# Kernel tuning notes

Measured on AMD Instinct MI355X. Metric: run time of the kernel, lower is better.

## Reference

```python
import jax, jax.numpy as jnp
import numpy as np

N = 8192
E = 262144


def gcn_layer(x, w, row, col, edge_weight, n_nodes):
    # support = x @ W ; out = A_sparse @ support (COO spmm via segment_sum)
    support = x @ w                              # [N, d_out]
    msg = support[col] * edge_weight[:, None]    # gather + scale, [E, d_out]
    return jax.ops.segment_sum(msg, row, num_segments=n_nodes)  # [N, d_out]


def setup_inputs() -> dict:
    key = jax.random.key(0)
    k1, k2, k3, k4, k5, k6 = jax.random.split(key, 6)
    x = jax.random.normal(k1, (N, 512), dtype=jnp.float32)
    w1 = jax.random.normal(k2, (512, 256), dtype=jnp.float32) * 0.05
    w2 = jax.random.normal(k3, (256, 16), dtype=jnp.float32) * 0.05
    edge_weight = jax.random.uniform(k4, (E,), dtype=jnp.float32)
    row = jax.random.randint(k5, (E,), 0, N, dtype=jnp.int32)
    col = jax.random.randint(k6, (E,), 0, N, dtype=jnp.int32)
    return {"x": x, "w1": w1, "w2": w2, "edge_weight": edge_weight,
            "row": row, "col": col}


def reference(x, w1, w2, edge_weight, row, col):
    # gc1: dropout(identity at eval) -> linear -> spmm -> relu
    h1 = jax.nn.relu(gcn_layer(x, w1, row, col, edge_weight, N))
    # gc2: identity activation
    z = gcn_layer(h1, w2, row, col, edge_weight, N)          # [N, 16]
    # InnerProductDecoder with act = identity (dropout off at eval)
    adj = z @ z.T                                            # [N, N]
    return adj
```

## Files before the change

### kernel.cpp

```cpp
#include <hip/hip_runtime.h>

#define NN 8192
#define NE 262144
#define DIN 512
#define DH 256
#define DZ 16
#define CAP 96

typedef __attribute__((ext_vector_type(8))) short bf16x8;
typedef __attribute__((ext_vector_type(4))) float f32x4;

__device__ __forceinline__ ushort f2bf(float f) {
    uint u = __float_as_uint(f);
    uint r = (u + 0x7FFFu + ((u >> 16) & 1u)) >> 16;
    return (ushort)r;
}
__device__ __forceinline__ float bf2f(ushort h) {
    return __uint_as_float((uint)h << 16);
}

__global__ __launch_bounds__(256) void k_gemm1_scatter(
    const float* __restrict__ X, const float* __restrict__ W1,
    ushort* __restrict__ O,
    const int* __restrict__ ROW, const int* __restrict__ COL,
    const float* __restrict__ EW, int* __restrict__ count,
    int* __restrict__ col_s, float* __restrict__ w_s) {
    __shared__ ushort As[32][72];
    __shared__ ushort Bs[256][72];
    int t = threadIdx.x;
    {
        int gid0 = blockIdx.x * 256 + t;
#pragma unroll
        for (int it = 0; it < 4; ++it) {
            int e = gid0 + it * 65536;
            int r = ROW[e];
            int slot = atomicAdd(&count[r], 1);
            if (slot < CAP) {
                col_s[r * CAP + slot] = COL[e];
                w_s[r * CAP + slot]   = EW[e];
            }
        }
    }
    int wave = t >> 6, lane = t & 63;
    int m0 = blockIdx.x * 32;
    int fr = lane & 15, fg = lane >> 4;
    int ar = t >> 3, ac = (t & 7) * 8;
    f32x4 acc[2][4] = {};
    for (int k0 = 0; k0 < DIN; k0 += 64) {
        __syncthreads();
        {
            const float* xp = &X[(size_t)(m0 + ar) * DIN + k0 + ac];
            float4 f0 = *(const float4*)&xp[0];
            float4 f1 = *(const float4*)&xp[4];
            ushort u[8] = {f2bf(f0.x), f2bf(f0.y), f2bf(f0.z), f2bf(f0.w),
                           f2bf(f1.x), f2bf(f1.y), f2bf(f1.z), f2bf(f1.w)};
            *(bf16x8*)&As[ar][ac] = *(const bf16x8*)&u[0];
        }
#pragma unroll
        for (int uix = 0; uix < 4; ++uix) {
            int u = uix * 256 + t;
            int kr = (u >> 6) * 4;
            int nc = (u & 63) * 4;
            const float* wp = &W1[(size_t)(k0 + kr) * DH + nc];
            float4 f0 = *(const float4*)&wp[0];
            float4 f1 = *(const float4*)&wp[DH];
            float4 f2 = *(const float4*)&wp[2 * DH];
            float4 f3 = *(const float4*)&wp[3 * DH];
            ushort4 p0 = {f2bf(f0.x), f2bf(f1.x), f2bf(f2.x), f2bf(f3.x)};
            ushort4 p1 = {f2bf(f0.y), f2bf(f1.y), f2bf(f2.y), f2bf(f3.y)};
            ushort4 p2 = {f2bf(f0.z), f2bf(f1.z), f2bf(f2.z), f2bf(f3.z)};
            ushort4 p3 = {f2bf(f0.w), f2bf(f1.w), f2bf(f2.w), f2bf(f3.w)};
            *(ushort4*)&Bs[nc + 0][kr] = p0;
            *(ushort4*)&Bs[nc + 1][kr] = p1;
            *(ushort4*)&Bs[nc + 2][kr] = p2;
            *(ushort4*)&Bs[nc + 3][kr] = p3;
        }
        __syncthreads();
#pragma unroll
        for (int kk = 0; kk < 2; ++kk) {
            bf16x8 af[2], bb[4];
#pragma unroll
            for (int i = 0; i < 2; ++i)
                af[i] = *(const bf16x8*)&As[i * 16 + fr][kk * 32 + fg * 8];
#pragma unroll
            for (int j = 0; j < 4; ++j)
                bb[j] = *(const bf16x8*)&Bs[wave * 64 + j * 16 + fr][kk * 32 + fg * 8];
#pragma unroll
            for (int i = 0; i < 2; ++i)
#pragma unroll
                for (int j = 0; j < 4; ++j)
                    acc[i][j] = __builtin_amdgcn_mfma_f32_16x16x32_bf16(
                        af[i], bb[j], acc[i][j], 0, 0, 0);
        }
    }
#pragma unroll
    for (int i = 0; i < 2; ++i)
#pragma unroll
        for (int j = 0; j < 4; ++j)
#pragma unroll
            for (int r = 0; r < 4; ++r)
                O[(size_t)(m0 + i * 16 + fg * 4 + r) * DH + wave * 64 + j * 16 + fr] =
                    f2bf(acc[i][j][r]);
}

__global__ __launch_bounds__(256) void k_spmm1_gemm2(const ushort* __restrict__ Sbf,
                                                     const int* __restrict__ count,
                                                     const int* __restrict__ cs,
                                                     const float* __restrict__ wsrt,
                                                     const float* __restrict__ W2,
                                                     float* __restrict__ S2) {
    __shared__ float w2s[DH * DZ];
    __shared__ float hs[2][DH];
    __shared__ int   ecs[2][CAP];
    __shared__ float ews[2][CAP];
    int t = threadIdx.x;
#pragma unroll
    for (int i = t; i < DH * DZ / 4; i += 256)
        ((float4*)w2s)[i] = ((const float4*)W2)[i];
    int sub = t >> 7;
    int ht = t & 127;
    int r = blockIdx.x * 2 + sub;
    int nv = min(count[r], CAP);
    int e0 = r * CAP;
    if (ht < nv) {
        ecs[sub][ht] = cs[e0 + ht];
        ews[sub][ht] = wsrt[e0 + ht];
    }
    float a0 = 0.f, a1 = 0.f, b0 = 0.f, b1 = 0.f;
    float c0 = 0.f, c1 = 0.f, d0 = 0.f, d1 = 0.f;
    __syncthreads();
    int e = 0;
    for (; e + 3 < nv; e += 4) {
        int k0 = ecs[sub][e], k1 = ecs[sub][e + 1], k2 = ecs[sub][e + 2], k3 = ecs[sub][e + 3];
        float w0 = ews[sub][e], w1 = ews[sub][e + 1], w2_ = ews[sub][e + 2], w3 = ews[sub][e + 3];
        uint p0 = *(const uint*)&Sbf[(size_t)k0 * DH + ht * 2];
        uint p1 = *(const uint*)&Sbf[(size_t)k1 * DH + ht * 2];
        uint p2 = *(const uint*)&Sbf[(size_t)k2 * DH + ht * 2];
        uint p3 = *(const uint*)&Sbf[(size_t)k3 * DH + ht * 2];
        a0 += w0 * bf2f((ushort)p0); a1 += w0 * bf2f((ushort)(p0 >> 16));
        b0 += w1 * bf2f((ushort)p1); b1 += w1 * bf2f((ushort)(p1 >> 16));
        c0 += w2_ * bf2f((ushort)p2); c1 += w2_ * bf2f((ushort)(p2 >> 16));
        d0 += w3 * bf2f((ushort)p3); d1 += w3 * bf2f((ushort)(p3 >> 16));
    }
    for (; e < nv; ++e) {
        float w0 = ews[sub][e];
        uint p0 = *(const uint*)&Sbf[(size_t)ecs[sub][e] * DH + ht * 2];
        a0 += w0 * bf2f((ushort)p0); a1 += w0 * bf2f((ushort)(p0 >> 16));
    }
    float2 o;
    o.x = fmaxf(a0 + b0 + c0 + d0, 0.f);
    o.y = fmaxf(a1 + b1 + c1 + d1, 0.f);
    *(float2*)&hs[sub][ht * 2] = o;
    __syncthreads();
    int j = (t >> 3) & 15, g = t & 7;
    float acc = 0.f;
#pragma unroll
    for (int kk = 0; kk < 32; ++kk) {
        int k = g * 32 + kk;
        acc += hs[sub][k] * w2s[k * DZ + j];
    }
    acc += __shfl_xor(acc, 1);
    acc += __shfl_xor(acc, 2);
    acc += __shfl_xor(acc, 4);
    if (g == 0) S2[(size_t)r * DZ + j] = acc;
}

__global__ __launch_bounds__(256) void k_spmm2(const float* __restrict__ S2,
                                               const int* __restrict__ count,
                                               const int* __restrict__ cs,
                                               const float* __restrict__ wsrt,
                                               ushort* __restrict__ ZHi,
                                               ushort* __restrict__ ZLo) {
    int t = threadIdx.x;
    int rl = t >> 4, c = t & 15;
    int r = blockIdx.x * 16 + rl;
    int nv = min(count[r], CAP);
    int e0 = r * CAP;
    float acc = 0.f;
    for (int e = 0; e < nv; ++e)
        acc += wsrt[e0 + e] * S2[(size_t)cs[e0 + e] * DZ + c];
    ushort h = f2bf(acc);
    ZHi[(size_t)r * DZ + c] = h;
    ZLo[(size_t)r * DZ + c] = f2bf(acc - bf2f(h));
}

__global__ __launch_bounds__(256) void k_gemm3_mfma(const ushort* __restrict__ ZHi,
                                                    const ushort* __restrict__ ZLo,
                                                    float* __restrict__ O) {
    int t = threadIdx.x;
    int wave = t >> 6, lane = t & 63;
    int rb = blockIdx.y * 128 + (wave >> 1) * 64;
    int cb = blockIdx.x * 128 + (wave & 1) * 64;
    int fr = lane & 15, fg = lane >> 4;
    int ko = (fg & 1) * 8;
    const ushort* asel = (fg < 2) ? ZHi : ZLo;

    bf16x8 cpack[4], rhi[4], rlo[4];
    bf16x8 zero8 = {};
#pragma unroll
    for (int j = 0; j < 4; ++j)
        cpack[j] = *(const bf16x8*)&asel[(size_t)(cb + j * 16 + fr) * DZ + ko];
#pragma unroll
    for (int i = 0; i < 4; ++i) {
        rhi[i] = *(const bf16x8*)&ZHi[(size_t)(rb + i * 16 + fr) * DZ + ko];
        rlo[i] = (fg < 2) ? *(const bf16x8*)&ZLo[(size_t)(rb + i * 16 + fr) * DZ + ko]
                          : zero8;
    }
    f32x4 acc[4][4] = {};
#pragma unroll
    for (int i = 0; i < 4; ++i)
#pragma unroll
        for (int j = 0; j < 4; ++j) {
            acc[i][j] = __builtin_amdgcn_mfma_f32_16x16x32_bf16(cpack[j], rhi[i],
                                                                acc[i][j], 0, 0, 0);
            acc[i][j] = __builtin_amdgcn_mfma_f32_16x16x32_bf16(cpack[j], rlo[i],
                                                                acc[i][j], 0, 0, 0);
        }
#pragma unroll
    for (int i = 0; i < 4; ++i)
#pragma unroll
        for (int j = 0; j < 4; ++j)
            *(f32x4*)&O[(size_t)(rb + i * 16 + fr) * NN + cb + j * 16 + fg * 4] = acc[i][j];
}

extern "C" void kernel_launch(void* const* d_in, const int* in_sizes, int n_in,
                              void* d_out, int out_size, void* d_ws, size_t ws_size,
                              hipStream_t stream) {
    const float* x  = (const float*)d_in[0];
    const float* w1 = (const float*)d_in[1];
    const float* w2 = (const float*)d_in[2];
    const float* ew = (const float*)d_in[3];
    const int*  row = (const int*)d_in[4];
    const int*  col = (const int*)d_in[5];
    float* out = (float*)d_out;

    char* ws = (char*)d_ws;
    int*    count = (int*)ws;
    ushort* zhi   = (ushort*)(ws + 73728);
    ushort* zlo   = (ushort*)(ws + 73728 + 262144);

    char* ob = (char*)d_out;
    ushort* support1 = (ushort*)ob;
    float*  s2       = (float*)(ob + 16u * 1024 * 1024);
    int*    col_s    = (int*)(ob + 24u * 1024 * 1024);
    float*  w_s      = (float*)(ob + 28u * 1024 * 1024);

    hipMemsetAsync(count, 0, NN * sizeof(int), stream);

    k_gemm1_scatter<<<NN / 32, 256, 0, stream>>>(x, w1, support1,
                                                 row, col, ew, count, col_s, w_s);
    k_spmm1_gemm2<<<NN / 2, 256, 0, stream>>>(support1, count, col_s, w_s, w2, s2);
    k_spmm2<<<NN / 16, 256, 0, stream>>>(s2, count, col_s, w_s, zhi, zlo);
    k_gemm3_mfma<<<dim3(NN / 128, NN / 128), 256, 0, stream>>>(zhi, zlo, out);
}
```

Before: 135.9 us.

## Pre-transpose W1 to bf16, drop LDS staging in GEMM1, wave-per-row SpMM1

A new prep kernel converts W1 to a transposed bf16 copy and zeroes the edge counters, replacing the memset. GEMM1 then reads MFMA operands directly from global memory with no LDS staging or barriers, using 16-row tiles and twice as many blocks. SpMM1 assigns one wave per row with 8-byte gathers and four rows per block. The aim is to remove the per-block redundant W1 conversion and transpose plus the LDS sync overhead, at the cost of more global or L2 traffic for B fragments and an extra launch.

```diff
diff --git a/kernel.cpp b/kernel.cpp
--- a/kernel.cpp
+++ b/kernel.cpp
@@ -19,20 +19,31 @@
     return __uint_as_float((uint)h << 16);
 }
 
+__global__ void k_prep_zero(const float* __restrict__ W, ushort* __restrict__ WBf,
+                            int* __restrict__ count) {
+    int b = blockIdx.x;
+    int t = threadIdx.x;
+    if (b < 512) {
+        int o = b * 256 + t;
+        int n = o >> 9, k = o & 511;
+        WBf[o] = f2bf(W[(size_t)k * DH + n]);
+    } else {
+        count[(b - 512) * 256 + t] = 0;
+    }
+}
+
 __global__ __launch_bounds__(256) void k_gemm1_scatter(
-    const float* __restrict__ X, const float* __restrict__ W1,
+    const float* __restrict__ X, const ushort* __restrict__ W1T,
     ushort* __restrict__ O,
     const int* __restrict__ ROW, const int* __restrict__ COL,
     const float* __restrict__ EW, int* __restrict__ count,
     int* __restrict__ col_s, float* __restrict__ w_s) {
-    __shared__ ushort As[32][72];
-    __shared__ ushort Bs[256][72];
     int t = threadIdx.x;
     {
         int gid0 = blockIdx.x * 256 + t;
 #pragma unroll
-        for (int it = 0; it < 4; ++it) {
-            int e = gid0 + it * 65536;
+        for (int it = 0; it < 2; ++it) {
+            int e = gid0 + it * 131072;
             int r = ROW[e];
             int slot = atomicAdd(&count[r], 1);
             if (slot < CAP) {
@@ -42,65 +53,32 @@
         }
     }
     int wave = t >> 6, lane = t & 63;
-    int m0 = blockIdx.x * 32;
+    int m0 = blockIdx.x * 16;
     int fr = lane & 15, fg = lane >> 4;
-    int ar = t >> 3, ac = (t & 7) * 8;
-    f32x4 acc[2][4] = {};
+    f32x4 acc[4] = {};
+    const float* xrow = &X[(size_t)(m0 + fr) * DIN];
     for (int k0 = 0; k0 < DIN; k0 += 64) {
-        __syncthreads();
-        {
-            const float* xp = &X[(size_t)(m0 + ar) * DIN + k0 + ac];
+#pragma unroll
+        for (int kk = 0; kk < 2; ++kk) {
+            const float* xp = &xrow[k0 + kk * 32 + fg * 8];
             float4 f0 = *(const float4*)&xp[0];
             float4 f1 = *(const float4*)&xp[4];
-            ushort u[8] = {f2bf(f0.x), f2bf(f0.y), f2bf(f0.z), f2bf(f0.w),
-                           f2bf(f1.x), f2bf(f1.y), f2bf(f1.z), f2bf(f1.w)};
-            *(bf16x8*)&As[ar][ac] = *(const bf16x8*)&u[0];
+            ushort ua[8] = {f2bf(f0.x), f2bf(f0.y), f2bf(f0.z), f2bf(f0.w),
+                            f2bf(f1.x), f2bf(f1.y), f2bf(f1.z), f2bf(f1.w)};
+            bf16x8 af = *(const bf16x8*)&ua[0];
+#pragma unroll
+            for (int j = 0; j < 4; ++j) {
+                bf16x8 bb = *(const bf16x8*)&W1T[(size_t)(wave * 64 + j * 16 + fr) * DIN +
+                                                 k0 + kk * 32 + fg * 8];
+                acc[j] = __builtin_amdgcn_mfma_f32_16x16x32_bf16(af, bb, acc[j], 0, 0, 0);
+            }
         }
-#pragma unroll
-        for (int uix = 0; uix < 4; ++uix) {
-            int u = uix * 256 + t;
-            int kr = (u >> 6) * 4;
-            int nc = (u & 63) * 4;
-            const float* wp = &W1[(size_t)(k0 + kr) * DH + nc];
-            float4 f0 = *(const float4*)&wp[0];
-            float4 f1 = *(const float4*)&wp[DH];
-            float4 f2 = *(const float4*)&wp[2 * DH];
-            float4 f3 = *(const float4*)&wp[3 * DH];
-            ushort4 p0 = {f2bf(f0.x), f2bf(f1.x), f2bf(f2.x), f2bf(f3.x)};
-            ushort4 p1 = {f2bf(f0.y), f2bf(f1.y), f2bf(f2.y), f2bf(f3.y)};
-            ushort4 p2 = {f2bf(f0.z), f2bf(f1.z), f2bf(f2.z), f2bf(f3.z)};
-            ushort4 p3 = {f2bf(f0.w), f2bf(f1.w), f2bf(f2.w), f2bf(f3.w)};
-            *(ushort4*)&Bs[nc + 0][kr] = p0;
-            *(ushort4*)&Bs[nc + 1][kr] = p1;
-            *(ushort4*)&Bs[nc + 2][kr] = p2;
-            *(ushort4*)&Bs[nc + 3][kr] = p3;
-        }
-        __syncthreads();
-#pragma unroll
-        for (int kk = 0; kk < 2; ++kk) {
-            bf16x8 af[2], bb[4];
-#pragma unroll
-            for (int i = 0; i < 2; ++i)
-                af[i] = *(const bf16x8*)&As[i * 16 + fr][kk * 32 + fg * 8];
-#pragma unroll
-            for (int j = 0; j < 4; ++j)
-                bb[j] = *(const bf16x8*)&Bs[wave * 64 + j * 16 + fr][kk * 32 + fg * 8];
-#pragma unroll
-            for (int i = 0; i < 2; ++i)
-#pragma unroll
-                for (int j = 0; j < 4; ++j)
-                    acc[i][j] = __builtin_amdgcn_mfma_f32_16x16x32_bf16(
-                        af[i], bb[j], acc[i][j], 0, 0, 0);
-        }
-    }
-#pragma unroll
-    for (int i = 0; i < 2; ++i)
-#pragma unroll
-        for (int j = 0; j < 4; ++j)
-#pragma unroll
-            for (int r = 0; r < 4; ++r)
-                O[(size_t)(m0 + i * 16 + fg * 4 + r) * DH + wave * 64 + j * 16 + fr] =
-                    f2bf(acc[i][j][r]);
+    }
+#pragma unroll
+    for (int j = 0; j < 4; ++j)
+#pragma unroll
+        for (int r = 0; r < 4; ++r)
+            O[(size_t)(m0 + fg * 4 + r) * DH + wave * 64 + j * 16 + fr] = f2bf(acc[j][r]);
 }
 
 __global__ __launch_bounds__(256) void k_spmm1_gemm2(const ushort* __restrict__ Sbf,
@@ -110,59 +88,61 @@
                                                      const float* __restrict__ W2,
                                                      float* __restrict__ S2) {
     __shared__ float w2s[DH * DZ];
-    __shared__ float hs[2][DH];
-    __shared__ int   ecs[2][CAP];
-    __shared__ float ews[2][CAP];
+    __shared__ float hs[4][DH];
+    __shared__ int   ecs[4][CAP];
+    __shared__ float ews[4][CAP];
     int t = threadIdx.x;
 #pragma unroll
     for (int i = t; i < DH * DZ / 4; i += 256)
         ((float4*)w2s)[i] = ((const float4*)W2)[i];
-    int sub = t >> 7;
-    int ht = t & 127;
-    int r = blockIdx.x * 2 + sub;
+    int wave = t >> 6, lane = t & 63;
+    int r = blockIdx.x * 4 + wave;
     int nv = min(count[r], CAP);
     int e0 = r * CAP;
-    if (ht < nv) {
-        ecs[sub][ht] = cs[e0 + ht];
-        ews[sub][ht] = wsrt[e0 + ht];
-    }
-    float a0 = 0.f, a1 = 0.f, b0 = 0.f, b1 = 0.f;
-    float c0 = 0.f, c1 = 0.f, d0 = 0.f, d1 = 0.f;
-    __syncthreads();
+    if (lane < nv) { ecs[wave][lane] = cs[e0 + lane]; ews[wave][lane] = wsrt[e0 + lane]; }
+    int l2 = lane + 64;
+    if (l2 < nv) { ecs[wave][l2] = cs[e0 + l2]; ews[wave][l2] = wsrt[e0 + l2]; }
+    float a0[4] = {}, a1[4] = {}, a2[4] = {}, a3[4] = {};
     int e = 0;
     for (; e + 3 < nv; e += 4) {
-        int k0 = ecs[sub][e], k1 = ecs[sub][e + 1], k2 = ecs[sub][e + 2], k3 = ecs[sub][e + 3];
-        float w0 = ews[sub][e], w1 = ews[sub][e + 1], w2_ = ews[sub][e + 2], w3 = ews[sub][e + 3];
-        uint p0 = *(const uint*)&Sbf[(size_t)k0 * DH + ht * 2];
-        uint p1 = *(const uint*)&Sbf[(size_t)k1 * DH + ht * 2];
-        uint p2 = *(const uint*)&Sbf[(size_t)k2 * DH + ht * 2];
-        uint p3 = *(const uint*)&Sbf[(size_t)k3 * DH + ht * 2];
-        a0 += w0 * bf2f((ushort)p0); a1 += w0 * bf2f((ushort)(p0 >> 16));
-        b0 += w1 * bf2f((ushort)p1); b1 += w1 * bf2f((ushort)(p1 >> 16));
-        c0 += w2_ * bf2f((ushort)p2); c1 += w2_ * bf2f((ushort)(p2 >> 16));
-        d0 += w3 * bf2f((ushort)p3); d1 += w3 * bf2f((ushort)(p3 >> 16));
+        int k0 = ecs[wave][e], k1 = ecs[wave][e + 1];
+        int k2 = ecs[wave][e + 2], k3 = ecs[wave][e + 3];
+        float w0 = ews[wave][e], w1 = ews[wave][e + 1];
+        float w2_ = ews[wave][e + 2], w3 = ews[wave][e + 3];
+        uint2 p0 = *(const uint2*)&Sbf[(size_t)k0 * DH + lane * 4];
+        uint2 p1 = *(const uint2*)&Sbf[(size_t)k1 * DH + lane * 4];
+        uint2 p2 = *(const uint2*)&Sbf[(size_t)k2 * DH + lane * 4];
+        uint2 p3 = *(const uint2*)&Sbf[(size_t)k3 * DH + lane * 4];
+        a0[0] += w0 * bf2f((ushort)p0.x); a0[1] += w0 * bf2f((ushort)(p0.x >> 16));
+        a0[2] += w0 * bf2f((ushort)p0.y); a0[3] += w0 * bf2f((ushort)(p0.y >> 16));
+        a1[0] += w1 * bf2f((ushort)p1.x); a1[1] += w1 * bf2f((ushort)(p1.x >> 16));
+        a1[2] += w1 * bf2f((ushort)p1.y); a1[3] += w1 * bf2f((ushort)(p1.y >> 16));
+        a2[0] += w2_ * bf2f((ushort)p2.x); a2[1] += w2_ * bf2f((ushort)(p2.x >> 16));
+        a2[2] += w2_ * bf2f((ushort)p2.y); a2[3] += w2_ * bf2f((ushort)(p2.y >> 16));
+        a3[0] += w3 * bf2f((ushort)p3.x); a3[1] += w3 * bf2f((ushort)(p3.x >> 16));
+        a3[2] += w3 * bf2f((ushort)p3.y); a3[3] += w3 * bf2f((ushort)(p3.y >> 16));
     }
     for (; e < nv; ++e) {
-        float w0 = ews[sub][e];
-        uint p0 = *(const uint*)&Sbf[(size_t)ecs[sub][e] * DH + ht * 2];
-        a0 += w0 * bf2f((ushort)p0); a1 += w0 * bf2f((ushort)(p0 >> 16));
-    }
-    float2 o;
-    o.x = fmaxf(a0 + b0 + c0 + d0, 0.f);
-    o.y = fmaxf(a1 + b1 + c1 + d1, 0.f);
-    *(float2*)&hs[sub][ht * 2] = o;
+        float w0 = ews[wave][e];
+        uint2 p0 = *(const uint2*)&Sbf[(size_t)ecs[wave][e] * DH + lane * 4];
+        a0[0] += w0 * bf2f((ushort)p0.x); a0[1] += w0 * bf2f((ushort)(p0.x >> 16));
+        a0[2] += w0 * bf2f((ushort)p0.y); a0[3] += w0 * bf2f((ushort)(p0.y >> 16));
+    }
+    float4 h;
+    h.x = fmaxf(a0[0] + a1[0] + a2[0] + a3[0], 0.f);
+    h.y = fmaxf(a0[1] + a1[1] + a2[1] + a3[1], 0.f);
+    h.z = fmaxf(a0[2] + a1[2] + a2[2] + a3[2], 0.f);
+    h.w = fmaxf(a0[3] + a1[3] + a2[3] + a3[3], 0.f);
+    *(float4*)&hs[wave][lane * 4] = h;
     __syncthreads();
-    int j = (t >> 3) & 15, g = t & 7;
+    int jj = lane >> 2, g = lane & 3;
     float acc = 0.f;
-#pragma unroll
-    for (int kk = 0; kk < 32; ++kk) {
-        int k = g * 32 + kk;
-        acc += hs[sub][k] * w2s[k * DZ + j];
-    }
+    int kb = g * 64;
+#pragma unroll 8
+    for (int k = kb; k < kb + 64; ++k) acc += hs[wave][k] * w2s[k * DZ + jj];
     acc += __shfl_xor(acc, 1);
     acc += __shfl_xor(acc, 2);
-    acc += __shfl_xor(acc, 4);
-    if (g == 0) S2[(size_t)r * DZ + j] = acc;
+    if (g == 0) S2[(size_t)r * DZ + jj] = acc;
 }
 
 __global__ __launch_bounds__(256) void k_spmm2(const float* __restrict__ S2,
@@ -244,12 +224,12 @@
     float*  s2       = (float*)(ob + 16u * 1024 * 1024);
     int*    col_s    = (int*)(ob + 24u * 1024 * 1024);
     float*  w_s      = (float*)(ob + 28u * 1024 * 1024);
-
-    hipMemsetAsync(count, 0, NN * sizeof(int), stream);
-
-    k_gemm1_scatter<<<NN / 32, 256, 0, stream>>>(x, w1, support1,
+    ushort* w1tbf    = (ushort*)(ob + 36u * 1024 * 1024);
+
+    k_prep_zero<<<544, 256, 0, stream>>>(w1, w1tbf, count);
+    k_gemm1_scatter<<<NN / 16, 256, 0, stream>>>(x, w1tbf, support1,
                                                  row, col, ew, count, col_s, w_s);
-    k_spmm1_gemm2<<<NN / 2, 256, 0, stream>>>(support1, count, col_s, w_s, w2, s2);
+    k_spmm1_gemm2<<<NN / 4, 256, 0, stream>>>(support1, count, col_s, w_s, w2, s2);
     k_spmm2<<<NN / 16, 256, 0, stream>>>(s2, count, col_s, w_s, zhi, zlo);
     k_gemm3_mfma<<<dim3(NN / 128, NN / 128), 256, 0, stream>>>(zhi, zlo, out);
 }
```

After: 133.0 us. 2.1% less time.
